# Kernel tuning notes

Measured on AMD Instinct MI355X. Metric: run time of the kernel, lower is better.

The kernel has to match this reference:

```python
import jax, jax.numpy as jnp
import numpy as np

B, F, V, D, H = 4096, 39, 100000, 16, 400


def setup_inputs() -> dict:
    key = jax.random.key(0)
    ks = jax.random.split(key, 8)
    Xi = jax.random.randint(ks[0], (B, F, 1), 0, V)
    Xv = jax.random.uniform(ks[1], (B, F, 1), dtype=jnp.float32)
    # per-feature embedding tables (all fea_sizes equal -> stacked)
    fst_tables = jax.random.normal(ks[2], (F, V, 1), dtype=jnp.float32)
    sec_tables = jax.random.normal(ks[3], (F, V, D), dtype=jnp.float32)
    # DNN: Linear(F*D -> H) + ReLU, Linear(H -> H) + ReLU
    W1 = jax.random.normal(ks[4], (F * D, H), dtype=jnp.float32) * 0.04
    b1 = jnp.zeros((H,), dtype=jnp.float32)
    W2 = jax.random.normal(ks[5], (H, H), dtype=jnp.float32) * 0.05
    b2 = jnp.zeros((H,), dtype=jnp.float32)
    bias = jax.random.normal(ks[6], (1,), dtype=jnp.float32)
    return dict(Xi=Xi, Xv=Xv, fst_tables=fst_tables, sec_tables=sec_tables,
                W1=W1, b1=b1, W2=W2, b2=b2, bias=bias)


def reference(Xi, Xv, fst_tables, sec_tables, W1, b1, W2, b2, bias):
    bsz, fnum, _ = Xi.shape
    idx = Xi[:, :, 0]                                  # [B,F] indices
    val = Xv[:, :, 0]                                  # [B,F] field values
    fr = jnp.arange(fnum)[None, :]                     # [1,F]
    # first-order: emb_i(Xi)*Xv summed over the length-1 axis -> [B,F]
    fst = fst_tables[fr, idx, 0] * val
    # second-order embeddings -> [B,F,D]
    sec = sec_tables[fr, idx] * val[:, :, None]
    # FM sum-of-squares trick: 0.5*((sum_f e)^2 - sum_f e^2) -> [B,D]
    s = sec.sum(axis=1)
    fm_sec = 0.5 * (s * s - (sec * sec).sum(axis=1))
    # DNN on flattened second-order embeddings
    sec_flat = sec.reshape(bsz, fnum * sec.shape[-1])  # [B, F*D]
    h = jax.nn.relu(sec_flat @ W1 + b1)
    deep = jax.nn.relu(h @ W2 + b2)                    # [B,H]
    return fst.sum(axis=1) + fm_sec.sum(axis=1) + bias + deep.sum(axis=1)
```

## Files before the change

kernel.cpp:

```cpp
#include <hip/hip_runtime.h>
#include <hip/hip_bf16.h>

#define B_SZ 4096
#define F_N  39
#define V_N  100000
#define D_N  16
#define H_N  400
#define K1   624
#define K1P  640
#define NP2  448

typedef __attribute__((ext_vector_type(8))) short short8;
typedef __attribute__((ext_vector_type(4))) float f32x4;

typedef const __attribute__((address_space(1))) void g_void;
typedef __attribute__((address_space(3))) void l_void;

#define GB       1024
#define W1_TILES (10 * 7)
#define W2_TILES (7 * 7)
#define PREP_GRID (GB + W1_TILES + W2_TILES + 1)

__global__ __launch_bounds__(256) void prep_kernel(
    const int*   __restrict__ Xi,
    const float* __restrict__ Xv,
    const float* __restrict__ fst_t,
    const float* __restrict__ sec_t,
    const float* __restrict__ bias,
    const float* __restrict__ W1, const float* __restrict__ b1,
    const float* __restrict__ W2, const float* __restrict__ b2,
    __hip_bfloat16* __restrict__ sec_flat,
    __hip_bfloat16* __restrict__ W1t, __hip_bfloat16* __restrict__ W2t,
    float* __restrict__ b1p, float* __restrict__ b2p,
    float* __restrict__ out)
{
    const int bid = blockIdx.x;
    const int tid = threadIdx.x;

    __shared__ float smem[4 * K1];
    __shared__ int   sidx4[4 * F_N];
    __shared__ float sval4[4 * F_N];
    __shared__ float ttile[64 * 65];

    if (bid < GB) {
        const int r = tid >> 6;
        const int l = tid & 63;

        if (tid < 4 * F_N) {
            sidx4[tid] = Xi[bid * (4 * F_N) + tid];
            sval4[tid] = Xv[bid * (4 * F_N) + tid];
        }
        __syncthreads();

        float4 gv[4];
        float  fv[4];
        #pragma unroll
        for (int it = 0; it < 4; ++it) {
            const int t = l + it * 64;
            gv[it] = make_float4(0.f, 0.f, 0.f, 0.f);
            fv[it] = 0.f;
            if (t < 156) {
                const int f = t >> 2, q = t & 3;
                gv[it] = *(const float4*)(sec_t +
                         ((long long)f * V_N + sidx4[r * F_N + f]) * D_N + q * 4);
            }
            if (t >= 156 && t < 156 + F_N) {
                const int ff = t - 156;
                fv[it] = fst_t[(long long)ff * V_N + sidx4[r * F_N + ff]];
            }
        }

        float ssq = 0.f, fstp = 0.f;
        #pragma unroll
        for (int it = 0; it < 4; ++it) {
            const int t = l + it * 64;
            if (t < 160) {
                float4 v = make_float4(0.f, 0.f, 0.f, 0.f);
                if (t < 156) {
                    const float val = sval4[r * F_N + (t >> 2)];
                    v.x = gv[it].x * val; v.y = gv[it].y * val;
                    v.z = gv[it].z * val; v.w = gv[it].w * val;
                    *(float4*)(smem + r * K1 + t * 4) = v;
                    ssq += v.x * v.x + v.y * v.y + v.z * v.z + v.w * v.w;
                }
                ushort4 pk;
                pk.x = __bfloat16_as_ushort(__float2bfloat16(v.x));
                pk.y = __bfloat16_as_ushort(__float2bfloat16(v.y));
                pk.z = __bfloat16_as_ushort(__float2bfloat16(v.z));
                pk.w = __bfloat16_as_ushort(__float2bfloat16(v.w));
                *(ushort4*)(sec_flat + (size_t)(bid * 4 + r) * K1P + t * 4) = pk;
            }
            if (t >= 156 && t < 156 + F_N)
                fstp += fv[it] * sval4[r * F_N + (t - 156)];
        }

        float part = fstp - 0.5f * ssq;
        if (l < D_N) {
            float sd = 0.f;
            #pragma unroll
            for (int f = 0; f < F_N; ++f)
                sd += smem[r * K1 + f * D_N + l];
            part += 0.5f * sd * sd;
        }
        #pragma unroll
        for (int off = 1; off < 64; off <<= 1)
            part += __shfl_xor(part, off, 64);
        if (l == 0) out[bid * 4 + r] = part + bias[0];
        return;
    }

    int tb = bid - GB;
    if (tb < W1_TILES + W2_TILES) {
        const float* Wsrc; __hip_bfloat16* Wdst;
        int Ksrc, Kdst, kb, nb2;
        if (tb < W1_TILES) { Wsrc = W1; Wdst = W1t; Ksrc = K1;  Kdst = K1P; kb = tb / 7; nb2 = tb % 7; }
        else { tb -= W1_TILES; Wsrc = W2; Wdst = W2t; Ksrc = H_N; Kdst = NP2; kb = tb / 7; nb2 = tb % 7; }
        const int k0 = kb * 64, n0 = nb2 * 64;
        #pragma unroll
        for (int p = 0; p < 4; ++p) {
            const int r  = (tid >> 4) + p * 16;
            const int c4 = (tid & 15) * 4;
            const int gk = k0 + r, gn = n0 + c4;
            float4 v = make_float4(0.f, 0.f, 0.f, 0.f);
            if (gk < Ksrc && gn + 3 < H_N)
                v = *(const float4*)(Wsrc + (size_t)gk * H_N + gn);
            ttile[(c4 + 0) * 65 + r] = v.x;
            ttile[(c4 + 1) * 65 + r] = v.y;
            ttile[(c4 + 2) * 65 + r] = v.z;
            ttile[(c4 + 3) * 65 + r] = v.w;
        }
        __syncthreads();
        const int rr = tid >> 2, cc = (tid & 3) * 16;
        short8 s0, s1;
        #pragma unroll
        for (int j = 0; j < 8; ++j) {
            s0[j] = (short)__bfloat16_as_ushort(__float2bfloat16(ttile[rr * 65 + cc + j]));
            s1[j] = (short)__bfloat16_as_ushort(__float2bfloat16(ttile[rr * 65 + cc + 8 + j]));
        }
        *(short8*)(Wdst + (size_t)(n0 + rr) * Kdst + k0 + cc)     = s0;
        *(short8*)(Wdst + (size_t)(n0 + rr) * Kdst + k0 + cc + 8) = s1;
        return;
    }

    if (tid < 256) {
        b1p[tid] = (tid < H_N) ? b1[tid] : 0.f;
        b2p[tid] = (tid < H_N) ? b2[tid] : 0.f;
        if (tid + 256 < NP2) {
            b1p[tid + 256] = (tid + 256 < H_N) ? b1[tid + 256] : 0.f;
            b2p[tid + 256] = (tid + 256 < H_N) ? b2[tid + 256] : 0.f;
        }
    }
}

template <int KT, bool ROWSUM>
__global__ __launch_bounds__(256) void mfma_gemm(
    const __hip_bfloat16* __restrict__ A,
    const __hip_bfloat16* __restrict__ Bt,
    const float* __restrict__ bias,
    __hip_bfloat16* __restrict__ C,
    float* __restrict__ out)
{
    __shared__ __align__(16) __hip_bfloat16 As[2][128 * 64];
    __shared__ __align__(16) __hip_bfloat16 Bs[2][64 * 64];

    const int tid  = threadIdx.x;
    const int lane = tid & 63;
    const int w    = tid >> 6;
    const int lr   = lane & 15;
    const int lg4  = lane >> 4;
    const int lk   = lg4 * 8;

    const int lin  = blockIdx.x;
    const int swz  = (lin & 7) * 28 + (lin >> 3);
    const int row0 = (swz / 7) * 128;
    const int col0 = (swz % 7) * 64;

    const int sr = tid >> 3;
    const int sc = (tid & 7) * 8;

    f32x4 acc[2][4] = {};

    auto STAGE = [&](int buf, int k0) {
        #pragma unroll
        for (int i = 0; i < 4; ++i)
            __builtin_amdgcn_global_load_lds(
                (g_void*)(A + (size_t)(row0 + sr + i * 32) * KT + k0 + sc),
                (l_void*)(&As[buf][(sr + i * 32) * 64 + sc]), 16, 0, 0);
        #pragma unroll
        for (int i = 0; i < 2; ++i)
            __builtin_amdgcn_global_load_lds(
                (g_void*)(Bt + (size_t)(col0 + sr + i * 32) * KT + k0 + sc),
                (l_void*)(&Bs[buf][(sr + i * 32) * 64 + sc]), 16, 0, 0);
    };

    constexpr int NT = KT / 64;
    STAGE(0, 0);
    __syncthreads();

    int cur = 0;
    for (int t = 0; t < NT; ++t) {
        if (t + 1 < NT) STAGE(cur ^ 1, (t + 1) * 64);
        #pragma unroll
        for (int ks = 0; ks < 2; ++ks) {
            short8 a[2], bb[4];
            #pragma unroll
            for (int m = 0; m < 2; ++m)
                a[m] = *(const short8*)(&As[cur][(w * 32 + m * 16 + lr) * 64 + ks * 32 + lk]);
            #pragma unroll
            for (int n = 0; n < 4; ++n)
                bb[n] = *(const short8*)(&Bs[cur][(n * 16 + lr) * 64 + ks * 32 + lk]);
            #pragma unroll
            for (int m = 0; m < 2; ++m)
                #pragma unroll
                for (int n = 0; n < 4; ++n)
                    acc[m][n] = __builtin_amdgcn_mfma_f32_16x16x32_bf16(
                        a[m], bb[n], acc[m][n], 0, 0, 0);
        }
        if (t + 1 < NT) {
            __syncthreads();
            cur ^= 1;
        }
    }

    if constexpr (!ROWSUM) {
        __syncthreads();
        float* ctile = (float*)&As[0][0];
        #pragma unroll
        for (int m = 0; m < 2; ++m) {
            const int rb = w * 32 + m * 16 + lg4 * 4;
            #pragma unroll
            for (int n = 0; n < 4; ++n) {
                const int col = n * 16 + lr;
                const float bv = bias[col0 + col];
                #pragma unroll
                for (int r = 0; r < 4; ++r)
                    ctile[(rb + r) * 64 + col] = fmaxf(acc[m][n][r] + bv, 0.f);
            }
        }
        __syncthreads();
        #pragma unroll
        for (int p = 0; p < 2; ++p) {
            const int row = (tid >> 2) + p * 64;
            const int cc  = (tid & 3) * 16;
            short8 s0, s1;
            #pragma unroll
            for (int j = 0; j < 8; ++j) {
                s0[j] = (short)__bfloat16_as_ushort(__float2bfloat16(ctile[row * 64 + cc + j]));
                s1[j] = (short)__bfloat16_as_ushort(__float2bfloat16(ctile[row * 64 + cc + 8 + j]));
            }
            *(short8*)(C + (size_t)(row0 + row) * NP2 + col0 + cc)     = s0;
            *(short8*)(C + (size_t)(row0 + row) * NP2 + col0 + cc + 8) = s1;
        }
    } else {
        #pragma unroll
        for (int m = 0; m < 2; ++m) {
            float v[4] = {0.f, 0.f, 0.f, 0.f};
            #pragma unroll
            for (int n = 0; n < 4; ++n) {
                const int col = col0 + n * 16 + lr;
                const float bv = bias[col];
                #pragma unroll
                for (int r = 0; r < 4; ++r)
                    v[r] += fmaxf(acc[m][n][r] + bv, 0.f);
            }
            #pragma unroll
            for (int off = 1; off < 16; off <<= 1)
                #pragma unroll
                for (int r = 0; r < 4; ++r)
                    v[r] += __shfl_xor(v[r], off, 64);
            if (lr == 0) {
                const int row = row0 + w * 32 + m * 16 + lg4 * 4;
                #pragma unroll
                for (int r = 0; r < 4; ++r)
                    atomicAdd(out + row + r, v[r]);
            }
        }
    }
}

extern "C" void kernel_launch(void* const* d_in, const int* in_sizes, int n_in,
                              void* d_out, int out_size, void* d_ws, size_t ws_size,
                              hipStream_t stream)
{
    const int*   Xi    = (const int*)  d_in[0];
    const float* Xv    = (const float*)d_in[1];
    const float* fst_t = (const float*)d_in[2];
    const float* sec_t = (const float*)d_in[3];
    const float* W1    = (const float*)d_in[4];
    const float* b1    = (const float*)d_in[5];
    const float* W2    = (const float*)d_in[6];
    const float* b2    = (const float*)d_in[7];
    const float* bias  = (const float*)d_in[8];

    float* out = (float*)d_out;
    char*  wsb = (char*)d_ws;

    __hip_bfloat16* sec_flat = (__hip_bfloat16*)(wsb);
    __hip_bfloat16* h        = (__hip_bfloat16*)(wsb + 5242880);
    __hip_bfloat16* W1t      = (__hip_bfloat16*)(wsb + 8912896);
    __hip_bfloat16* W2t      = (__hip_bfloat16*)(wsb + 9486336);
    float*          b1p      = (float*)(wsb + 9887744);
    float*          b2p      = (float*)(wsb + 9889536);

    prep_kernel<<<PREP_GRID, 256, 0, stream>>>(
        Xi, Xv, fst_t, sec_t, bias, W1, b1, W2, b2,
        sec_flat, W1t, W2t, b1p, b2p, out);

    mfma_gemm<K1P, false><<<224, 256, 0, stream>>>(sec_flat, W1t, b1p, h, nullptr);
    mfma_gemm<NP2, true ><<<224, 256, 0, stream>>>(h, W2t, b2p, nullptr, out);
}
```

Before: 37.28 us.

## Use 64x64 GEMM tiles, triple-buffered LDS pipeline, and XOR-swizzled operand layout

The GEMM tile shrinks from 128x64 to 64x64 with a 2x2 wave layout, doubling the grid to 448 blocks so more CUs are busy. The two-stage double buffer becomes a three-stage ring with explicit vmcnt waits and raw barriers, so loads run two tiles ahead. Producers write sec_flat, the transposed weights and the hidden activations in XOR-swizzled 16-byte chunks, letting the direct global-to-LDS copies land in a bank-conflict-free layout. Bias values are loaded once into registers. Smaller tiles lower per-block data reuse, and the hand-written waitcnt counts must match the number of loads in flight.

New measurement: 31.08 us. 16.6% less time.

```diff
diff --git a/kernel.cpp b/kernel.cpp
--- a/kernel.cpp
+++ b/kernel.cpp
@@ -20,6 +20,7 @@
 #define W1_TILES (10 * 7)
 #define W2_TILES (7 * 7)
 #define PREP_GRID (GB + W1_TILES + W2_TILES + 1)
+
 
 __global__ __launch_bounds__(256) void prep_kernel(
     const int*   __restrict__ Xi,
@@ -70,6 +71,7 @@
             }
         }
 
+        const int grow = bid * 4 + r;
         float ssq = 0.f, fstp = 0.f;
         #pragma unroll
         for (int it = 0; it < 4; ++it) {
@@ -88,7 +90,9 @@
                 pk.y = __bfloat16_as_ushort(__float2bfloat16(v.y));
                 pk.z = __bfloat16_as_ushort(__float2bfloat16(v.z));
                 pk.w = __bfloat16_as_ushort(__float2bfloat16(v.w));
-                *(ushort4*)(sec_flat + (size_t)(bid * 4 + r) * K1P + t * 4) = pk;
+                const int ch = t >> 1;
+                const int cs = (ch & ~7) | ((ch ^ grow) & 7);
+                *(ushort4*)(sec_flat + (size_t)grow * K1P + cs * 8 + (t & 1) * 4) = pk;
             }
             if (t >= 156 && t < 156 + F_N)
                 fstp += fv[it] * sval4[r * F_N + (t - 156)];
@@ -105,7 +109,7 @@
         #pragma unroll
         for (int off = 1; off < 64; off <<= 1)
             part += __shfl_xor(part, off, 64);
-        if (l == 0) out[bid * 4 + r] = part + bias[0];
+        if (l == 0) out[grow] = part + bias[0];
         return;
     }
 
@@ -131,14 +135,19 @@
         }
         __syncthreads();
         const int rr = tid >> 2, cc = (tid & 3) * 16;
+        const int n  = n0 + rr;
         short8 s0, s1;
         #pragma unroll
         for (int j = 0; j < 8; ++j) {
             s0[j] = (short)__bfloat16_as_ushort(__float2bfloat16(ttile[rr * 65 + cc + j]));
             s1[j] = (short)__bfloat16_as_ushort(__float2bfloat16(ttile[rr * 65 + cc + 8 + j]));
         }
-        *(short8*)(Wdst + (size_t)(n0 + rr) * Kdst + k0 + cc)     = s0;
-        *(short8*)(Wdst + (size_t)(n0 + rr) * Kdst + k0 + cc + 8) = s1;
+        const int c0  = (k0 + cc) >> 3;
+        const int c1  = c0 + 1;
+        const int c0s = (c0 & ~7) | ((c0 ^ n) & 7);
+        const int c1s = (c1 & ~7) | ((c1 ^ n) & 7);
+        *(short8*)(Wdst + (size_t)n * Kdst + c0s * 8) = s0;
+        *(short8*)(Wdst + (size_t)n * Kdst + c1s * 8) = s1;
         return;
     }
 
@@ -160,65 +169,77 @@
     __hip_bfloat16* __restrict__ C,
     float* __restrict__ out)
 {
-    __shared__ __align__(16) __hip_bfloat16 As[2][128 * 64];
-    __shared__ __align__(16) __hip_bfloat16 Bs[2][64 * 64];
+    __shared__ __align__(16) __hip_bfloat16 As[3][64 * 64];
+    __shared__ __align__(16) __hip_bfloat16 Bs[3][64 * 64];
 
     const int tid  = threadIdx.x;
     const int lane = tid & 63;
-    const int w    = tid >> 6;
+    const int wid  = tid >> 6;
+    const int wm   = wid >> 1;
+    const int wn   = wid & 1;
     const int lr   = lane & 15;
     const int lg4  = lane >> 4;
-    const int lk   = lg4 * 8;
 
     const int lin  = blockIdx.x;
-    const int swz  = (lin & 7) * 28 + (lin >> 3);
-    const int row0 = (swz / 7) * 128;
+    const int swz  = (lin & 7) * 56 + (lin >> 3);
+    const int row0 = (swz / 7) * 64;
     const int col0 = (swz % 7) * 64;
 
     const int sr = tid >> 3;
     const int sc = (tid & 7) * 8;
 
-    f32x4 acc[2][4] = {};
+    float bvv[2];
+    #pragma unroll
+    for (int n = 0; n < 2; ++n)
+        bvv[n] = bias[col0 + wn * 32 + n * 16 + lr];
+    asm volatile("" :: "v"(bvv[0]), "v"(bvv[1]));
+    asm volatile("s_waitcnt vmcnt(0)" ::: "memory");
 
     auto STAGE = [&](int buf, int k0) {
         #pragma unroll
-        for (int i = 0; i < 4; ++i)
+        for (int i = 0; i < 2; ++i) {
             __builtin_amdgcn_global_load_lds(
-                (g_void*)(A + (size_t)(row0 + sr + i * 32) * KT + k0 + sc),
-                (l_void*)(&As[buf][(sr + i * 32) * 64 + sc]), 16, 0, 0);
-        #pragma unroll
-        for (int i = 0; i < 2; ++i)
+                (g_void*)(A + (size_t)(row0 + i * 32 + sr) * KT + k0 + sc),
+                (l_void*)(&As[buf][(i * 32 + sr) * 64 + sc]), 16, 0, 0);
             __builtin_amdgcn_global_load_lds(
-                (g_void*)(Bt + (size_t)(col0 + sr + i * 32) * KT + k0 + sc),
-                (l_void*)(&Bs[buf][(sr + i * 32) * 64 + sc]), 16, 0, 0);
+                (g_void*)(Bt + (size_t)(col0 + i * 32 + sr) * KT + k0 + sc),
+                (l_void*)(&Bs[buf][(i * 32 + sr) * 64 + sc]), 16, 0, 0);
+        }
     };
 
     constexpr int NT = KT / 64;
     STAGE(0, 0);
-    __syncthreads();
-
-    int cur = 0;
+    STAGE(1, 64);
+
+    f32x4 acc[2][2] = {};
     for (int t = 0; t < NT; ++t) {
-        if (t + 1 < NT) STAGE(cur ^ 1, (t + 1) * 64);
+        if (t + 1 < NT) asm volatile("s_waitcnt vmcnt(4)" ::: "memory");
+        else            asm volatile("s_waitcnt vmcnt(0)" ::: "memory");
+        __builtin_amdgcn_s_barrier();
+        if (t + 2 < NT) STAGE((t + 2) % 3, (t + 2) * 64);
+
+        const int cb = t % 3;
         #pragma unroll
         for (int ks = 0; ks < 2; ++ks) {
-            short8 a[2], bb[4];
+            short8 a[2], bb[2];
+            #pragma unroll
+            for (int m = 0; m < 2; ++m) {
+                const int row = wm * 32 + m * 16 + lr;
+                const int ch  = (ks * 4 + lg4) ^ (row & 7);
+                a[m] = *(const short8*)(&As[cb][row * 64 + ch * 8]);
+            }
+            #pragma unroll
+            for (int n = 0; n < 2; ++n) {
+                const int row = wn * 32 + n * 16 + lr;
+                const int ch  = (ks * 4 + lg4) ^ (row & 7);
+                bb[n] = *(const short8*)(&Bs[cb][row * 64 + ch * 8]);
+            }
             #pragma unroll
             for (int m = 0; m < 2; ++m)
-                a[m] = *(const short8*)(&As[cur][(w * 32 + m * 16 + lr) * 64 + ks * 32 + lk]);
-            #pragma unroll
-            for (int n = 0; n < 4; ++n)
-                bb[n] = *(const short8*)(&Bs[cur][(n * 16 + lr) * 64 + ks * 32 + lk]);
-            #pragma unroll
-            for (int m = 0; m < 2; ++m)
-                #pragma unroll
-                for (int n = 0; n < 4; ++n)
+                #pragma unroll
+                for (int n = 0; n < 2; ++n)
                     acc[m][n] = __builtin_amdgcn_mfma_f32_16x16x32_bf16(
                         a[m], bb[n], acc[m][n], 0, 0, 0);
-        }
-        if (t + 1 < NT) {
-            __syncthreads();
-            cur ^= 1;
         }
     }
 
@@ -227,41 +248,39 @@
         float* ctile = (float*)&As[0][0];
         #pragma unroll
         for (int m = 0; m < 2; ++m) {
-            const int rb = w * 32 + m * 16 + lg4 * 4;
-            #pragma unroll
-            for (int n = 0; n < 4; ++n) {
-                const int col = n * 16 + lr;
-                const float bv = bias[col0 + col];
+            const int rb = wm * 32 + m * 16 + lg4 * 4;
+            #pragma unroll
+            for (int n = 0; n < 2; ++n) {
+                const int col = wn * 32 + n * 16 + lr;
                 #pragma unroll
                 for (int r = 0; r < 4; ++r)
-                    ctile[(rb + r) * 64 + col] = fmaxf(acc[m][n][r] + bv, 0.f);
+                    ctile[(rb + r) * 64 + col] = fmaxf(acc[m][n][r] + bvv[n], 0.f);
             }
         }
         __syncthreads();
-        #pragma unroll
-        for (int p = 0; p < 2; ++p) {
-            const int row = (tid >> 2) + p * 64;
-            const int cc  = (tid & 3) * 16;
-            short8 s0, s1;
-            #pragma unroll
-            for (int j = 0; j < 8; ++j) {
-                s0[j] = (short)__bfloat16_as_ushort(__float2bfloat16(ctile[row * 64 + cc + j]));
-                s1[j] = (short)__bfloat16_as_ushort(__float2bfloat16(ctile[row * 64 + cc + 8 + j]));
-            }
-            *(short8*)(C + (size_t)(row0 + row) * NP2 + col0 + cc)     = s0;
-            *(short8*)(C + (size_t)(row0 + row) * NP2 + col0 + cc + 8) = s1;
-        }
+        const int row = tid >> 2;
+        const int cc  = (tid & 3) * 16;
+        short8 s0, s1;
+        #pragma unroll
+        for (int j = 0; j < 8; ++j) {
+            s0[j] = (short)__bfloat16_as_ushort(__float2bfloat16(ctile[row * 64 + cc + j]));
+            s1[j] = (short)__bfloat16_as_ushort(__float2bfloat16(ctile[row * 64 + cc + 8 + j]));
+        }
+        const int c0  = (col0 + cc) >> 3;
+        const int c1  = c0 + 1;
+        const int c0s = (c0 & ~7) | ((c0 ^ row) & 7);
+        const int c1s = (c1 & ~7) | ((c1 ^ row) & 7);
+        *(short8*)(C + (size_t)(row0 + row) * NP2 + c0s * 8) = s0;
+        *(short8*)(C + (size_t)(row0 + row) * NP2 + c1s * 8) = s1;
     } else {
         #pragma unroll
         for (int m = 0; m < 2; ++m) {
             float v[4] = {0.f, 0.f, 0.f, 0.f};
             #pragma unroll
-            for (int n = 0; n < 4; ++n) {
-                const int col = col0 + n * 16 + lr;
-                const float bv = bias[col];
+            for (int n = 0; n < 2; ++n) {
                 #pragma unroll
                 for (int r = 0; r < 4; ++r)
-                    v[r] += fmaxf(acc[m][n][r] + bv, 0.f);
+                    v[r] += fmaxf(acc[m][n][r] + bvv[n], 0.f);
             }
             #pragma unroll
             for (int off = 1; off < 16; off <<= 1)
@@ -269,7 +288,7 @@
                 for (int r = 0; r < 4; ++r)
                     v[r] += __shfl_xor(v[r], off, 64);
             if (lr == 0) {
-                const int row = row0 + w * 32 + m * 16 + lg4 * 4;
+                const int row = row0 + wm * 32 + m * 16 + lg4 * 4;
                 #pragma unroll
                 for (int r = 0; r < 4; ++r)
                     atomicAdd(out + row + r, v[r]);
@@ -306,6 +325,6 @@
         Xi, Xv, fst_t, sec_t, bias, W1, b1, W2, b2,
         sec_flat, W1t, W2t, b1p, b2p, out);
 
-    mfma_gemm<K1P, false><<<224, 256, 0, stream>>>(sec_flat, W1t, b1p, h, nullptr);
-    mfma_gemm<NP2, true ><<<224, 256, 0, stream>>>(h, W2t, b2p, nullptr, out);
+    mfma_gemm<K1P, false><<<448, 256, 0, stream>>>(sec_flat, W1t, b1p, h, nullptr);
+    mfma_gemm<NP2, true ><<<448, 256, 0, stream>>>(h, W2t, b2p, nullptr, out);
 }
```
